# Kernel optimization log

Measured on AMD Instinct MI355X. Metric: run time of the kernel, lower is better.

## Reference

```python
import jax, jax.numpy as jnp
import numpy as np

SIGMA = 0.2
BN_EPS = 1e-5


def setup_inputs() -> dict:
    key = jax.random.key(0)
    k1, k2, k3, k4 = jax.random.split(key, 4)
    B, N, K = 8, 16384, 64
    normals = jax.random.normal(k1, (B, 3, N), dtype=jnp.float32)
    # normalize to unit normals (faithful to what the module consumes in practice)
    normals = normals / jnp.linalg.norm(normals, axis=1, keepdims=True)
    neighbor_idx = jax.random.randint(k2, (B, N, 3), 0, N, dtype=jnp.int64)
    weight_alpha = jax.random.uniform(k3, (1, K, 4), dtype=jnp.float32) * np.pi
    weight_beta = jax.random.uniform(k4, (1, K, 4), dtype=jnp.float32) * (2 * np.pi)
    bn_gamma = jnp.ones((K,), dtype=jnp.float32)
    bn_beta = jnp.zeros((K,), dtype=jnp.float32)
    return {
        "normals": normals,
        "neighbor_idx": neighbor_idx,
        "weight_alpha": weight_alpha,
        "weight_beta": weight_beta,
        "bn_gamma": bn_gamma,
        "bn_beta": bn_beta,
    }


def reference(normals, neighbor_idx, weight_alpha, weight_beta, bn_gamma, bn_beta):
    # normals: (B, 3, N); neighbor_idx: (B, N, 3)
    # kernel directions on unit sphere: W[c, k, m], c in xyz, m in 4 points per kernel
    W = jnp.concatenate(
        [
            jnp.sin(weight_alpha) * jnp.cos(weight_beta),
            jnp.sin(weight_alpha) * jnp.sin(weight_beta),
            jnp.cos(weight_alpha),
        ],
        axis=0,
    )  # (3, K, 4)

    # gather neighbor normals: nbr[b, c, i, j] = normals[b, c, neighbor_idx[b, i, j]]
    nbr = jax.vmap(lambda nm, idx: nm[:, idx])(normals, neighbor_idx)  # (B, 3, N, 3)
    F = jnp.concatenate([normals[:, :, :, None], nbr], axis=3)  # (B, 3, N, 4) face points p

    # squared distances via ||f||^2 + ||w||^2 - 2 f.w  (avoids 6D broadcast of torch code)
    dots = jnp.einsum("bcnp,ckm->bknpm", F, W)  # (B, K, N, 4, 4)
    F2 = jnp.sum(F * F, axis=1)[:, None, :, :, None]  # (B, 1, N, 4, 1)
    W2 = jnp.sum(W * W, axis=0)[None, :, None, None, :]  # (1, K, 1, 1, 4)
    dist = F2 + W2 - 2.0 * dots  # (B, K, N, 4, 4)

    inv = -1.0 / (2.0 * SIGMA * SIGMA)
    feat = jnp.sum(jnp.exp(dist * inv), axis=(3, 4)) / 16.0  # (B, K, N)

    # BatchNorm1d (training mode, biased variance over batch+spatial dims) + ReLU
    mean = jnp.mean(feat, axis=(0, 2), keepdims=True)
    var = jnp.var(feat, axis=(0, 2), keepdims=True)
    xhat = (feat - mean) * jax.lax.rsqrt(var + BN_EPS)
    out = bn_gamma[None, :, None] * xhat + bn_beta[None, :, None]
    return jax.nn.relu(out)
```

## Files before the change

### kernel.cpp

```cpp
#include <hip/hip_runtime.h>

#define BB 8
#define NN 16384
#define KK 64

#if __has_builtin(__builtin_amdgcn_exp2f)
#define EXP2(x) __builtin_amdgcn_exp2f(x)
#else
#define EXP2(x) exp2f(x)
#endif

#define LOG2E 1.44269504088896340736f
#define CW (25.0f * LOG2E)
#define CE (-12.5f * LOG2E)

__global__ __launch_bounds__(256) void fkc_prep(
    const float* __restrict__ walpha, const float* __restrict__ wbeta,
    float* __restrict__ wx, float* __restrict__ wy, float* __restrict__ wz)
{
    const int t = threadIdx.x;
    float a = walpha[t];
    float b = wbeta[t];
    float sa = __sinf(a);
    wx[t] = CW * sa * __cosf(b);
    wy[t] = CW * sa * __sinf(b);
    wz[t] = CW * __cosf(a);
}

__global__ __launch_bounds__(256, 8) void fkc_main(
    const float* __restrict__ normals,
    const int*   __restrict__ nidx,
    const float* __restrict__ wx, const float* __restrict__ wy,
    const float* __restrict__ wz,
    float* __restrict__ out)
{
    const int tid = threadIdx.x;
    const int pg = blockIdx.x >> 2;
    const int k0 = (blockIdx.x & 3) * 16;
    const int gid = pg * 256 + tid;
    const int b = gid >> 14;
    const int n = gid & (NN - 1);
    const float* nb = normals + b * 3 * NN;

    float fx[4], fy[4], fz[4], e2[4];
    fx[0] = nb[n];
    fy[0] = nb[NN + n];
    fz[0] = nb[2 * NN + n];
    const int ibase = (b * NN + n) * 3;
#pragma unroll
    for (int j = 0; j < 3; ++j) {
        int id = nidx[ibase + j];
        fx[j + 1] = nb[id];
        fy[j + 1] = nb[NN + id];
        fz[j + 1] = nb[2 * NN + id];
    }
#pragma unroll
    for (int p = 0; p < 4; ++p) {
        float n2 = fmaf(fx[p], fx[p], fmaf(fy[p], fy[p], fz[p] * fz[p]));
        e2[p] = CE * (n2 + 1.0f);
    }

    float* orow = out + (b * KK + k0) * NN + n;
#pragma unroll
    for (int kk = 0; kk < 16; ++kk) {
        float acc = 0.0f;
#pragma unroll
        for (int m = 0; m < 4; ++m) {
            const int wi = ((k0 + kk) << 2) + m;
            float wxv = wx[wi], wyv = wy[wi], wzv = wz[wi];
#pragma unroll
            for (int p = 0; p < 4; ++p) {
                float arg = fmaf(fz[p], wzv,
                            fmaf(fy[p], wyv,
                            fmaf(fx[p], wxv, e2[p])));
                acc += EXP2(arg);
            }
        }
        orow[kk * NN] = acc;
    }
}

__global__ __launch_bounds__(256) void fkc_reduce(
    const float4* __restrict__ out4,
    float* __restrict__ psum,
    float* __restrict__ pss)
{
    __shared__ float sw[4], ssw[4];
    const int tid = threadIdx.x;
    const int k = blockIdx.x >> 2;
    const int c = blockIdx.x & 3;

    float s = 0.0f, ss = 0.0f;
#pragma unroll
    for (int r = 0; r < 2; ++r) {
        const int b = 2 * c + r;
        const int base4 = (b * KK + k) * (NN / 4);
#pragma unroll
        for (int j = 0; j < 16; ++j) {
            float4 v = out4[base4 + tid + j * 256];
            s += (v.x + v.y) + (v.z + v.w);
            ss += fmaf(v.x, v.x, fmaf(v.y, v.y, fmaf(v.z, v.z, v.w * v.w)));
        }
    }
#pragma unroll
    for (int off = 1; off < 64; off <<= 1) {
        s  += __shfl_xor(s,  off, 64);
        ss += __shfl_xor(ss, off, 64);
    }
    const int wv = tid >> 6;
    if ((tid & 63) == 0) { sw[wv] = s; ssw[wv] = ss; }
    __syncthreads();
    if (tid == 0) {
        psum[k * 4 + c] = sw[0] + sw[1] + sw[2] + sw[3];
        pss[k * 4 + c]  = ssw[0] + ssw[1] + ssw[2] + ssw[3];
    }
}

__global__ __launch_bounds__(256) void fkc_apply(
    float4* __restrict__ out4,
    const float* __restrict__ psum,
    const float* __restrict__ pss,
    const float* __restrict__ gamma,
    const float* __restrict__ beta)
{
    const int i = blockIdx.x * 256 + threadIdx.x;
    const int k = (i >> 12) & (KK - 1);

    float st  = (psum[k * 4 + 0] + psum[k * 4 + 1]) +
                (psum[k * 4 + 2] + psum[k * 4 + 3]);
    float sst = (pss[k * 4 + 0] + pss[k * 4 + 1]) +
                (pss[k * 4 + 2] + pss[k * 4 + 3]);
    const float invM = 1.0f / (float)(BB * NN);
    float mean = st * invM;
    float var = fmaf(-mean, mean, sst * invM);
    float sc = gamma[k] * rsqrtf(var + 1e-5f);
    float sh = fmaf(-mean, sc, beta[k]);

    float4 v = out4[i];
    v.x = fmaxf(fmaf(v.x, sc, sh), 0.0f);
    v.y = fmaxf(fmaf(v.y, sc, sh), 0.0f);
    v.z = fmaxf(fmaf(v.z, sc, sh), 0.0f);
    v.w = fmaxf(fmaf(v.w, sc, sh), 0.0f);
    out4[i] = v;
}

extern "C" void kernel_launch(void* const* d_in, const int* in_sizes, int n_in,
                              void* d_out, int out_size, void* d_ws, size_t ws_size,
                              hipStream_t stream) {
    const float* normals = (const float*)d_in[0];
    const int*   nidx    = (const int*)d_in[1];
    const float* walpha  = (const float*)d_in[2];
    const float* wbeta   = (const float*)d_in[3];
    const float* gamma   = (const float*)d_in[4];
    const float* beta    = (const float*)d_in[5];
    float* out = (float*)d_out;
    float* ws = (float*)d_ws;

    float* psum = ws;
    float* pss  = ws + 256;
    float* wxb  = ws + 512;
    float* wyb  = ws + 768;
    float* wzb  = ws + 1024;

    fkc_prep<<<1, 256, 0, stream>>>(walpha, wbeta, wxb, wyb, wzb);
    fkc_main<<<2048, 256, 0, stream>>>(normals, nidx, wxb, wyb, wzb, out);
    fkc_reduce<<<256, 256, 0, stream>>>((const float4*)out, psum, pss);
    fkc_apply<<<8192, 256, 0, stream>>>((float4*)out, psum, pss, gamma, beta);
}
```

Measured before the change: 116.6 us.

## Fuse BN statistics into main kernel via atomics and use packed v2f FMAs

The separate reduction kernel that re-read the whole output to compute per-channel sum and sum of squares is removed. The main kernel now reduces its 256x16 tile through LDS and atomically adds the partial sums into global accumulators, which are zeroed with a memset. The distance arithmetic is also rewritten with two-wide float vectors so the compiler can emit packed FMA instructions. This saves one full 32 MB read pass and a launch, at the cost of extra LDS traffic, barriers and float atomics whose summation order is nondeterministic.

```diff
diff --git a/kernel.cpp b/kernel.cpp
--- a/kernel.cpp
+++ b/kernel.cpp
@@ -8,6 +8,16 @@
 #define EXP2(x) __builtin_amdgcn_exp2f(x)
 #else
 #define EXP2(x) exp2f(x)
+#endif
+
+typedef float v2f __attribute__((ext_vector_type(2)));
+
+#if __has_builtin(__builtin_elementwise_fma)
+#define FMA2(a, b, c) __builtin_elementwise_fma((a), (b), (c))
+#else
+static __device__ inline v2f FMA2(v2f a, v2f b, v2f c) {
+    v2f r; r.x = fmaf(a.x, b.x, c.x); r.y = fmaf(a.y, b.y, c.y); return r;
+}
 #endif
 
 #define LOG2E 1.44269504088896340736f
@@ -32,8 +42,13 @@
     const int*   __restrict__ nidx,
     const float* __restrict__ wx, const float* __restrict__ wy,
     const float* __restrict__ wz,
-    float* __restrict__ out)
+    float* __restrict__ out,
+    float* __restrict__ gsum,
+    float* __restrict__ gss)
 {
+    __shared__ float fl[16][257];
+    __shared__ float ps[16][17], pq[16][17];
+
     const int tid = threadIdx.x;
     const int pg = blockIdx.x >> 2;
     const int k0 = (blockIdx.x & 3) * 16;
@@ -42,7 +57,7 @@
     const int n = gid & (NN - 1);
     const float* nb = normals + b * 3 * NN;
 
-    float fx[4], fy[4], fz[4], e2[4];
+    float fx[4], fy[4], fz[4];
     fx[0] = nb[n];
     fy[0] = nb[NN + n];
     fz[0] = nb[2 * NN + n];
@@ -54,85 +69,83 @@
         fy[j + 1] = nb[NN + id];
         fz[j + 1] = nb[2 * NN + id];
     }
-#pragma unroll
-    for (int p = 0; p < 4; ++p) {
-        float n2 = fmaf(fx[p], fx[p], fmaf(fy[p], fy[p], fz[p] * fz[p]));
-        e2[p] = CE * (n2 + 1.0f);
+
+    v2f fx01 = {fx[0], fx[1]}, fx23 = {fx[2], fx[3]};
+    v2f fy01 = {fy[0], fy[1]}, fy23 = {fy[2], fy[3]};
+    v2f fz01 = {fz[0], fz[1]}, fz23 = {fz[2], fz[3]};
+    v2f e01, e23;
+    {
+        v2f n2a = FMA2(fx01, fx01, FMA2(fy01, fy01, fz01 * fz01));
+        v2f n2b = FMA2(fx23, fx23, FMA2(fy23, fy23, fz23 * fz23));
+        e01 = CE * (n2a + 1.0f);
+        e23 = CE * (n2b + 1.0f);
     }
 
     float* orow = out + (b * KK + k0) * NN + n;
 #pragma unroll
     for (int kk = 0; kk < 16; ++kk) {
-        float acc = 0.0f;
+        v2f acc01 = {0.0f, 0.0f}, acc23 = {0.0f, 0.0f};
 #pragma unroll
         for (int m = 0; m < 4; ++m) {
             const int wi = ((k0 + kk) << 2) + m;
             float wxv = wx[wi], wyv = wy[wi], wzv = wz[wi];
+            v2f wx2 = {wxv, wxv}, wy2 = {wyv, wyv}, wz2 = {wzv, wzv};
+            v2f a01 = FMA2(fz01, wz2, FMA2(fy01, wy2, FMA2(fx01, wx2, e01)));
+            v2f a23 = FMA2(fz23, wz2, FMA2(fy23, wy2, FMA2(fx23, wx2, e23)));
+            v2f x01 = {EXP2(a01.x), EXP2(a01.y)};
+            v2f x23 = {EXP2(a23.x), EXP2(a23.y)};
+            acc01 += x01;
+            acc23 += x23;
+        }
+        v2f t2 = acc01 + acc23;
+        float acc = t2.x + t2.y;
+        orow[kk * NN] = acc;
+        fl[kk][tid] = acc;
+    }
+    __syncthreads();
+
+    {
+        const int k = tid & 15;
+        const int part = tid >> 4;
+        float s = 0.0f, ss = 0.0f;
 #pragma unroll
-            for (int p = 0; p < 4; ++p) {
-                float arg = fmaf(fz[p], wzv,
-                            fmaf(fy[p], wyv,
-                            fmaf(fx[p], wxv, e2[p])));
-                acc += EXP2(arg);
-            }
+        for (int r = 0; r < 16; ++r) {
+            float v = fl[k][part * 16 + r];
+            s += v;
+            ss = fmaf(v, v, ss);
         }
-        orow[kk * NN] = acc;
+        ps[k][part] = s;
+        pq[k][part] = ss;
     }
-}
+    __syncthreads();
 
-__global__ __launch_bounds__(256) void fkc_reduce(
-    const float4* __restrict__ out4,
-    float* __restrict__ psum,
-    float* __restrict__ pss)
-{
-    __shared__ float sw[4], ssw[4];
-    const int tid = threadIdx.x;
-    const int k = blockIdx.x >> 2;
-    const int c = blockIdx.x & 3;
-
-    float s = 0.0f, ss = 0.0f;
+    if (tid < 16) {
+        float s = 0.0f;
 #pragma unroll
-    for (int r = 0; r < 2; ++r) {
-        const int b = 2 * c + r;
-        const int base4 = (b * KK + k) * (NN / 4);
+        for (int r = 0; r < 16; ++r) s += ps[tid][r];
+        atomicAdd(&gsum[k0 + tid], s);
+    } else if (tid < 32) {
+        const int kk = tid - 16;
+        float ss = 0.0f;
 #pragma unroll
-        for (int j = 0; j < 16; ++j) {
-            float4 v = out4[base4 + tid + j * 256];
-            s += (v.x + v.y) + (v.z + v.w);
-            ss += fmaf(v.x, v.x, fmaf(v.y, v.y, fmaf(v.z, v.z, v.w * v.w)));
-        }
-    }
-#pragma unroll
-    for (int off = 1; off < 64; off <<= 1) {
-        s  += __shfl_xor(s,  off, 64);
-        ss += __shfl_xor(ss, off, 64);
-    }
-    const int wv = tid >> 6;
-    if ((tid & 63) == 0) { sw[wv] = s; ssw[wv] = ss; }
-    __syncthreads();
-    if (tid == 0) {
-        psum[k * 4 + c] = sw[0] + sw[1] + sw[2] + sw[3];
-        pss[k * 4 + c]  = ssw[0] + ssw[1] + ssw[2] + ssw[3];
+        for (int r = 0; r < 16; ++r) ss += pq[kk][r];
+        atomicAdd(&gss[k0 + kk], ss);
     }
 }
 
 __global__ __launch_bounds__(256) void fkc_apply(
     float4* __restrict__ out4,
-    const float* __restrict__ psum,
-    const float* __restrict__ pss,
+    const float* __restrict__ gsum,
+    const float* __restrict__ gss,
     const float* __restrict__ gamma,
     const float* __restrict__ beta)
 {
     const int i = blockIdx.x * 256 + threadIdx.x;
     const int k = (i >> 12) & (KK - 1);
 
-    float st  = (psum[k * 4 + 0] + psum[k * 4 + 1]) +
-                (psum[k * 4 + 2] + psum[k * 4 + 3]);
-    float sst = (pss[k * 4 + 0] + pss[k * 4 + 1]) +
-                (pss[k * 4 + 2] + pss[k * 4 + 3]);
     const float invM = 1.0f / (float)(BB * NN);
-    float mean = st * invM;
-    float var = fmaf(-mean, mean, sst * invM);
+    float mean = gsum[k] * invM;
+    float var = fmaf(-mean, mean, gss[k] * invM);
     float sc = gamma[k] * rsqrtf(var + 1e-5f);
     float sh = fmaf(-mean, sc, beta[k]);
 
@@ -156,14 +169,16 @@
     float* out = (float*)d_out;
     float* ws = (float*)d_ws;
 
-    float* psum = ws;
-    float* pss  = ws + 256;
-    float* wxb  = ws + 512;
-    float* wyb  = ws + 768;
-    float* wzb  = ws + 1024;
+    float* gsum = ws;
+    float* gss  = ws + 64;
+    float* wxb  = ws + 128;
+    float* wyb  = ws + 384;
+    float* wzb  = ws + 640;
+
+    hipMemsetAsync(ws, 0, 128 * sizeof(float), stream);
 
     fkc_prep<<<1, 256, 0, stream>>>(walpha, wbeta, wxb, wyb, wzb);
-    fkc_main<<<2048, 256, 0, stream>>>(normals, nidx, wxb, wyb, wzb, out);
-    fkc_reduce<<<256, 256, 0, stream>>>((const float4*)out, psum, pss);
-    fkc_apply<<<8192, 256, 0, stream>>>((float4*)out, psum, pss, gamma, beta);
+    fkc_main<<<2048, 256, 0, stream>>>(normals, nidx, wxb, wyb, wzb,
+                                       out, gsum, gss);
+    fkc_apply<<<8192, 256, 0, stream>>>((float4*)out, gsum, gss, gamma, beta);
 }
```

Result: faster. 111.1 us (median of 2 runs) (-4.7%).
